# Performance work log

Hardware: AMD Instinct MI355X
Metric: run time of the kernel (lower is better)

Reference implementation:

```python
import jax, jax.numpy as jnp
import numpy as np

B = 8192
D_LS, D_A, D_LM, D_AT, D_DS, D_DM = 1024, 512, 512, 512, 1024, 512
LENGTH = D_LS + D_A + D_LM  # 2048
OUT = 512


def setup_inputs() -> dict:
    key = jax.random.key(0)
    ks = jax.random.split(key, 9)
    return {
        "result_ls": jax.random.normal(ks[0], (B, 1, D_LS), jnp.float32),
        "result_A": jax.random.normal(ks[1], (B, 1, D_A), jnp.float32),
        "result_lm": jax.random.normal(ks[2], (B, 1, D_LM), jnp.float32),
        "result_AT": jax.random.normal(ks[3], (B, 1, D_AT), jnp.float32),
        "result_ds": jax.random.normal(ks[4], (B, 1, D_DS), jnp.float32),
        "result_dm": jax.random.normal(ks[5], (B, 1, D_DM), jnp.float32),
        "W": jax.random.normal(ks[6], (OUT, LENGTH), jnp.float32) * (1.0 / np.sqrt(LENGTH)),
        "b": jax.random.normal(ks[7], (OUT,), jnp.float32) * 0.01,
        "h_n": jax.random.normal(ks[8], (OUT, 1), jnp.float32) * (1.0 / np.sqrt(OUT)),
    }


def _pad_to(x, length):
    # zero-pad last dim of [B,1,d] to [B,1,length]
    return jnp.pad(x, ((0, 0), (0, 0), (0, length - x.shape[2])))


def reference(result_ls, result_A, result_lm, result_AT, result_ds, result_dm, W, b, h_n):
    # pad each node-type feature to common length and stack along node axis -> [B,6,L]
    nodes = jnp.concatenate(
        [_pad_to(t, LENGTH) for t in (result_ls, result_A, result_lm, result_AT, result_ds, result_dm)],
        axis=1,
    )
    temp = jnp.tanh(jnp.einsum("bnl,ol->bno", nodes, W) + b)  # [B,6,OUT]
    score = jnp.einsum("bno,oi->bni", temp, h_n)               # [B,6,1]
    score = score.reshape(-1, 1, 6)
    beta = jax.nn.softmax(score, axis=2)                        # [B,1,6]
    z_i = jnp.matmul(beta, nodes)                               # [B,1,L]
    return z_i
```

## Files before the change

kernel.cpp:

```cpp
#include <hip/hip_runtime.h>
#include <hip/hip_bf16.h>
#include <stdint.h>

typedef __attribute__((ext_vector_type(8))) short bf16x8;
typedef __attribute__((ext_vector_type(4))) float f32x4;

#define NB 8192

__device__ __forceinline__ unsigned pkbf(float x, float y) {
    __hip_bfloat162 h = __float22bfloat162_rn(make_float2(x, y));
    unsigned r;
    __builtin_memcpy(&r, &h, 4);
    return r;
}

__device__ __forceinline__ uint4 pack8(float4 a, float4 b) {
    uint4 r;
    r.x = pkbf(a.x, a.y);
    r.y = pkbf(a.z, a.w);
    r.z = pkbf(b.x, b.y);
    r.w = pkbf(b.z, b.w);
    return r;
}

__global__ __launch_bounds__(256)
void prep_w_kernel(const float* __restrict__ W, uint4* __restrict__ Wt) {
    int t = blockIdx.x * 256 + threadIdx.x;
    int lane = t & 63;
    int frag = t >> 6;
    int kb = frag >> 5, cb = frag & 31;
    int o = cb * 16 + (lane & 15);
    int k = kb * 32 + ((lane >> 4) << 3);
    const float* src = W + (size_t)o * 2048 + k;
    float4 a = *(const float4*)src;
    float4 b = *(const float4*)(src + 4);
    Wt[t] = pack8(a, b);
}

template<int MFN, int DN>
__device__ __forceinline__ void score_body(
        const float* __restrict__ xp, int node, int m0,
        const float* __restrict__ bias, const float* __restrict__ hvec,
        const uint4* __restrict__ Wt, float* __restrict__ scores,
        uint4* lA, float* red) {
    constexpr int BM = MFN * 16;
    constexpr int NKB = DN / 32;
    int t = threadIdx.x;
    int l = t & 63;
    int w = t >> 6;

#pragma unroll
    for (int j = 0; j < 16; ++j) {
        int f = (t >> 6) + j * 8;
        int kb = f / MFN, mf = f % MFN;
        int row = mf * 16 + (l & 15);
        int k = kb * 32 + ((l >> 4) << 3);
        const float* g = xp + (size_t)(m0 + row) * DN + k;
        float4 a = *(const float4*)g;
        float4 b = *(const float4*)(g + 4);
        lA[f * 64 + l] = pack8(a, b);
    }
    __syncthreads();

    f32x4 acc[MFN][4];
#pragma unroll
    for (int mf = 0; mf < MFN; ++mf)
#pragma unroll
        for (int nf = 0; nf < 4; ++nf)
            acc[mf][nf] = (f32x4){0.f, 0.f, 0.f, 0.f};

    bf16x8 bcur[4];
    {
        const uint4* wp = Wt + ((0 + (w << 2)) << 6) + l;
#pragma unroll
        for (int nf = 0; nf < 4; ++nf) {
            uint4 u = wp[nf << 6];
            __builtin_memcpy(&bcur[nf], &u, 16);
        }
    }
    for (int kb = 0; kb < NKB; ++kb) {
        bf16x8 bnxt[4];
        if (kb + 1 < NKB) {
            const uint4* wp = Wt + ((((kb + 1) << 5) + (w << 2)) << 6) + l;
#pragma unroll
            for (int nf = 0; nf < 4; ++nf) {
                uint4 u = wp[nf << 6];
                __builtin_memcpy(&bnxt[nf], &u, 16);
            }
        }
#pragma unroll
        for (int mf = 0; mf < MFN; ++mf) {
            uint4 u = lA[(kb * MFN + mf) * 64 + l];
            bf16x8 afr;
            __builtin_memcpy(&afr, &u, 16);
#pragma unroll
            for (int nf = 0; nf < 4; ++nf)
                acc[mf][nf] = __builtin_amdgcn_mfma_f32_16x16x32_bf16(
                    afr, bcur[nf], acc[mf][nf], 0, 0, 0);
        }
#pragma unroll
        for (int nf = 0; nf < 4; ++nf) bcur[nf] = bnxt[nf];
    }

    float bv[4], hv[4];
#pragma unroll
    for (int nf = 0; nf < 4; ++nf) {
        int o = (w << 6) + (nf << 4) + (l & 15);
        bv[nf] = bias[o];
        hv[nf] = hvec[o];
    }
#pragma unroll
    for (int mf = 0; mf < MFN; ++mf) {
        float sc[4] = {0.f, 0.f, 0.f, 0.f};
#pragma unroll
        for (int nf = 0; nf < 4; ++nf) {
#pragma unroll
            for (int r = 0; r < 4; ++r) {
                float xv = acc[mf][nf][r] + bv[nf];
                float th = 1.f - 2.f * __builtin_amdgcn_rcpf(1.f + __expf(2.f * xv));
                sc[r] = fmaf(hv[nf], th, sc[r]);
            }
        }
#pragma unroll
        for (int r = 0; r < 4; ++r) {
            float v = sc[r];
            v += __shfl_xor(v, 1);
            v += __shfl_xor(v, 2);
            v += __shfl_xor(v, 4);
            v += __shfl_xor(v, 8);
            if ((l & 15) == 0)
                red[w * BM + (mf << 4) + ((l >> 4) << 2) + r] = v;
        }
    }
    __syncthreads();
    if (t < BM) {
        float ssum = 0.f;
#pragma unroll
        for (int w2 = 0; w2 < 8; ++w2) ssum += red[w2 * BM + t];
        scores[node * NB + m0 + t] = ssum;
    }
}

__global__ __launch_bounds__(512, 2)
void score_kernel(const float* __restrict__ x0, const float* __restrict__ x1,
                  const float* __restrict__ x2, const float* __restrict__ x3,
                  const float* __restrict__ x4, const float* __restrict__ x5,
                  const float* __restrict__ bias, const float* __restrict__ hvec,
                  const uint4* __restrict__ Wt, float* __restrict__ scores) {
    __shared__ uint4 lA[8192];
    __shared__ float red[8 * 128];

    int bid = blockIdx.x;
    if (bid < 256) {
        const float* xp = (bid & 1) ? x4 : x0;
        int node = (bid & 1) ? 4 : 0;
        int m0 = (bid >> 1) * 64;
        score_body<4, 1024>(xp, node, m0, bias, hvec, Wt, scores, lA, red);
    } else {
        int lb = bid - 256;
        int ni = lb & 3;
        const float* xp = (ni == 0) ? x1 : (ni == 1) ? x2 : (ni == 2) ? x3 : x5;
        int node = (ni == 0) ? 1 : (ni == 1) ? 2 : (ni == 2) ? 3 : 5;
        int m0 = (lb >> 2) * 128;
        score_body<8, 512>(xp, node, m0, bias, hvec, Wt, scores, lA, red);
    }
}

__global__ __launch_bounds__(256)
void z_kernel(const float* __restrict__ x0, const float* __restrict__ x1,
              const float* __restrict__ x2, const float* __restrict__ x3,
              const float* __restrict__ x4, const float* __restrict__ x5,
              const float* __restrict__ scores, float* __restrict__ out) {
    int wv = threadIdx.x >> 6;
    int lane = threadIdx.x & 63;
    int b = (blockIdx.x << 2) + wv;

    float s0 = scores[b];
    float s1 = scores[NB + b];
    float s2 = scores[2 * NB + b];
    float s3 = scores[3 * NB + b];
    float s4 = scores[4 * NB + b];
    float s5 = scores[5 * NB + b];
    float m = fmaxf(fmaxf(fmaxf(s0, s1), fmaxf(s2, s3)), fmaxf(s4, s5));
    float e0 = __expf(s0 - m), e1 = __expf(s1 - m), e2 = __expf(s2 - m);
    float e3 = __expf(s3 - m), e4 = __expf(s4 - m), e5 = __expf(s5 - m);
    float inv = __builtin_amdgcn_rcpf(e0 + e1 + e2 + e3 + e4 + e5);
    float b0 = e0 * inv, b1 = e1 * inv, b2 = e2 * inv;
    float b3 = e3 * inv, b4 = e4 * inv, b5 = e5 * inv;

    const float* pls = x0 + (size_t)b * 1024;
    const float* pA  = x1 + (size_t)b * 512;
    const float* plm = x2 + (size_t)b * 512;
    const float* pAT = x3 + (size_t)b * 512;
    const float* pds = x4 + (size_t)b * 1024;
    const float* pdm = x5 + (size_t)b * 512;
    float* po = out + (size_t)b * 2048;

#pragma unroll
    for (int j = 0; j < 2; ++j) {
        int c = (j << 8) + (lane << 2);
        float4 vls = *(const float4*)(pls + c);
        float4 vA  = *(const float4*)(pA + c);
        float4 vlm = *(const float4*)(plm + c);
        float4 vAT = *(const float4*)(pAT + c);
        float4 vds = *(const float4*)(pds + c);
        float4 vdm = *(const float4*)(pdm + c);
        float4 r;
        r.x = b0*vls.x + b1*vA.x + b2*vlm.x + b3*vAT.x + b4*vds.x + b5*vdm.x;
        r.y = b0*vls.y + b1*vA.y + b2*vlm.y + b3*vAT.y + b4*vds.y + b5*vdm.y;
        r.z = b0*vls.z + b1*vA.z + b2*vlm.z + b3*vAT.z + b4*vds.z + b5*vdm.z;
        r.w = b0*vls.w + b1*vA.w + b2*vlm.w + b3*vAT.w + b4*vds.w + b5*vdm.w;
        *(float4*)(po + c) = r;
    }
#pragma unroll
    for (int j = 0; j < 2; ++j) {
        int c = 512 + (j << 8) + (lane << 2);
        float4 vls = *(const float4*)(pls + c);
        float4 vds = *(const float4*)(pds + c);
        float4 r;
        r.x = b0*vls.x + b4*vds.x;
        r.y = b0*vls.y + b4*vds.y;
        r.z = b0*vls.z + b4*vds.z;
        r.w = b0*vls.w + b4*vds.w;
        *(float4*)(po + c) = r;
    }
    float4 zz = make_float4(0.f, 0.f, 0.f, 0.f);
#pragma unroll
    for (int j = 0; j < 4; ++j) {
        int c = 1024 + (j << 8) + (lane << 2);
        *(float4*)(po + c) = zz;
    }
}

extern "C" void kernel_launch(void* const* d_in, const int* in_sizes, int n_in,
                              void* d_out, int out_size, void* d_ws, size_t ws_size,
                              hipStream_t stream) {
    const float* x0   = (const float*)d_in[0];
    const float* x1   = (const float*)d_in[1];
    const float* x2   = (const float*)d_in[2];
    const float* x3   = (const float*)d_in[3];
    const float* x4   = (const float*)d_in[4];
    const float* x5   = (const float*)d_in[5];
    const float* W    = (const float*)d_in[6];
    const float* bias = (const float*)d_in[7];
    const float* hvec = (const float*)d_in[8];

    uint4* Wt = (uint4*)d_ws;
    float* scores = (float*)((char*)d_ws + (1u << 20));

    prep_w_kernel<<<256, 256, 0, stream>>>(W, Wt);
    score_kernel<<<512, 512, 0, stream>>>(x0, x1, x2, x3, x4, x5, bias, hvec, Wt, scores);
    z_kernel<<<2048, 256, 0, stream>>>(x0, x1, x2, x3, x4, x5, scores, (float*)d_out);
}
```

Baseline: 94.36 us.

## Pre-pack activations to bf16 fragment layout and stream them into LDS asynchronously

A new pre-pass converts all six activation tensors to bf16 in MFMA fragment order in the workspace. The score kernel then copies tiles straight into LDS with global_load_lds, uses 64-row tiles with half the LDS, and raises occupancy to 4 blocks per CU over 768 blocks. The aim is to take the fp32 conversion and scattered loads off the GEMM's critical path and raise occupancy. The cost is an extra 32 MB bf16 write and read-back, and the W-fragment prefetch double buffering is dropped. The old path is kept as a fallback when the workspace is too small.

New measurement: 131.3 us. +39.2%, slower.

```diff
diff --git a/kernel.cpp b/kernel.cpp
--- a/kernel.cpp
+++ b/kernel.cpp
@@ -21,6 +21,12 @@
     r.z = pkbf(b.x, b.y);
     r.w = pkbf(b.z, b.w);
     return r;
+}
+
+__device__ __forceinline__ void gload16(const uint4* g, void* l) {
+    __builtin_amdgcn_global_load_lds(
+        (const __attribute__((address_space(1))) void*)g,
+        (__attribute__((address_space(3))) void*)l, 16, 0, 0);
 }
 
 __global__ __launch_bounds__(256)
@@ -32,13 +38,149 @@
     int o = cb * 16 + (lane & 15);
     int k = kb * 32 + ((lane >> 4) << 3);
     const float* src = W + (size_t)o * 2048 + k;
-    float4 a = *(const float4*)src;
-    float4 b = *(const float4*)(src + 4);
-    Wt[t] = pack8(a, b);
+    Wt[t] = pack8(*(const float4*)src, *(const float4*)(src + 4));
+}
+
+__global__ __launch_bounds__(256)
+void prep_a_kernel(const float* __restrict__ x0, const float* __restrict__ x1,
+                   const float* __restrict__ x2, const float* __restrict__ x3,
+                   const float* __restrict__ x4, const float* __restrict__ x5,
+                   uint4* __restrict__ A) {
+    int c = blockIdx.x * 256 + threadIdx.x;
+    int s = c >> 19;
+    const float* xp; int dn, cn, cshift;
+    if (s < 2)      { xp = x0; dn = 1024; cn = c;                 cshift = 13; }
+    else if (s == 2){ xp = x1; dn = 512;  cn = c - (2 << 19);     cshift = 12; }
+    else if (s == 3){ xp = x2; dn = 512;  cn = c - (3 << 19);     cshift = 12; }
+    else if (s == 4){ xp = x3; dn = 512;  cn = c - (4 << 19);     cshift = 12; }
+    else if (s < 7) { xp = x4; dn = 1024; cn = c - (5 << 19);     cshift = 13; }
+    else            { xp = x5; dn = 512;  cn = c - (7 << 19);     cshift = 12; }
+    int tile = cn >> cshift;
+    int cc = cn & ((1 << cshift) - 1);
+    int f = cc >> 6, l = cc & 63;
+    int kb = f >> 2, mf = f & 3;
+    int row = (tile << 6) + (mf << 4) + (l & 15);
+    int k = (kb << 5) + ((l >> 4) << 3);
+    const float* src = xp + (size_t)row * dn + k;
+    A[c] = pack8(*(const float4*)src, *(const float4*)(src + 4));
+}
+
+template<int DN>
+__device__ __forceinline__ void score_v10_body(
+        const uint4* __restrict__ an, int node, int tile,
+        const float* __restrict__ bias, const float* __restrict__ hvec,
+        const uint4* __restrict__ Wt, float* __restrict__ scores,
+        uint4* lA, float* red) {
+    constexpr int NKH = DN / 512;
+    constexpr int CPT = DN * 8;
+    int t = threadIdx.x;
+    int l = t & 63;
+    int w = t >> 6;
+
+    f32x4 acc[4][4];
+#pragma unroll
+    for (int mf = 0; mf < 4; ++mf)
+#pragma unroll
+        for (int nf = 0; nf < 4; ++nf)
+            acc[mf][nf] = (f32x4){0.f, 0.f, 0.f, 0.f};
+
+    const uint4* tbase = an + (size_t)tile * CPT;
+
+    for (int kh = 0; kh < NKH; ++kh) {
+        if (kh > 0) __syncthreads();
+        {
+            const uint4* sb = tbase + (kh << 12) + (w << 9);
+            char* db = (char*)lA + ((w << 9) << 4);
+#pragma unroll
+            for (int i = 0; i < 8; ++i)
+                gload16(sb + (i << 6) + l, db + (i << 10));
+        }
+        __syncthreads();
+
+        for (int kbh = 0; kbh < 16; ++kbh) {
+            int kb = (kh << 4) + kbh;
+            const uint4* wp = Wt + (((kb << 5) + (w << 2)) << 6) + l;
+            bf16x8 bfr[4];
+#pragma unroll
+            for (int nf = 0; nf < 4; ++nf) {
+                uint4 u = wp[nf << 6];
+                __builtin_memcpy(&bfr[nf], &u, 16);
+            }
+#pragma unroll
+            for (int mf = 0; mf < 4; ++mf) {
+                uint4 u = lA[(((kbh << 2) + mf) << 6) + l];
+                bf16x8 afr;
+                __builtin_memcpy(&afr, &u, 16);
+#pragma unroll
+                for (int nf = 0; nf < 4; ++nf)
+                    acc[mf][nf] = __builtin_amdgcn_mfma_f32_16x16x32_bf16(
+                        afr, bfr[nf], acc[mf][nf], 0, 0, 0);
+            }
+        }
+    }
+
+    float bv[4], hv[4];
+#pragma unroll
+    for (int nf = 0; nf < 4; ++nf) {
+        int o = (w << 6) + (nf << 4) + (l & 15);
+        bv[nf] = bias[o];
+        hv[nf] = hvec[o];
+    }
+#pragma unroll
+    for (int mf = 0; mf < 4; ++mf) {
+        float sc[4] = {0.f, 0.f, 0.f, 0.f};
+#pragma unroll
+        for (int nf = 0; nf < 4; ++nf) {
+#pragma unroll
+            for (int r = 0; r < 4; ++r) {
+                float xv = acc[mf][nf][r] + bv[nf];
+                float th = 1.f - 2.f * __builtin_amdgcn_rcpf(1.f + __expf(2.f * xv));
+                sc[r] = fmaf(hv[nf], th, sc[r]);
+            }
+        }
+#pragma unroll
+        for (int r = 0; r < 4; ++r) {
+            float v = sc[r];
+            v += __shfl_xor(v, 1);
+            v += __shfl_xor(v, 2);
+            v += __shfl_xor(v, 4);
+            v += __shfl_xor(v, 8);
+            if ((l & 15) == 0)
+                red[(w << 6) + (mf << 4) + ((l >> 4) << 2) + r] = v;
+        }
+    }
+    __syncthreads();
+    if (t < 64) {
+        float ssum = 0.f;
+#pragma unroll
+        for (int w2 = 0; w2 < 8; ++w2) ssum += red[(w2 << 6) + t];
+        scores[node * NB + (tile << 6) + t] = ssum;
+    }
+}
+
+__global__ __launch_bounds__(512, 4)
+void score_v10_kernel(const uint4* __restrict__ a0, const uint4* __restrict__ a1,
+                      const uint4* __restrict__ a2, const uint4* __restrict__ a3,
+                      const uint4* __restrict__ a4, const uint4* __restrict__ a5,
+                      const float* __restrict__ bias, const float* __restrict__ hvec,
+                      const uint4* __restrict__ Wt, float* __restrict__ scores) {
+    __shared__ uint4 lA[4096];
+    __shared__ float red[8 * 64];
+    int bid = blockIdx.x;
+    int node = bid % 6;
+    int tile = bid / 6;
+    switch (node) {
+        case 0: score_v10_body<1024>(a0, 0, tile, bias, hvec, Wt, scores, lA, red); break;
+        case 1: score_v10_body<512>(a1, 1, tile, bias, hvec, Wt, scores, lA, red); break;
+        case 2: score_v10_body<512>(a2, 2, tile, bias, hvec, Wt, scores, lA, red); break;
+        case 3: score_v10_body<512>(a3, 3, tile, bias, hvec, Wt, scores, lA, red); break;
+        case 4: score_v10_body<1024>(a4, 4, tile, bias, hvec, Wt, scores, lA, red); break;
+        default: score_v10_body<512>(a5, 5, tile, bias, hvec, Wt, scores, lA, red); break;
+    }
 }
 
 template<int MFN, int DN>
-__device__ __forceinline__ void score_body(
+__device__ __forceinline__ void fb_score_body(
         const float* __restrict__ xp, int node, int m0,
         const float* __restrict__ bias, const float* __restrict__ hvec,
         const uint4* __restrict__ Wt, float* __restrict__ scores,
@@ -48,7 +190,6 @@
     int t = threadIdx.x;
     int l = t & 63;
     int w = t >> 6;
-
 #pragma unroll
     for (int j = 0; j < 16; ++j) {
         int f = (t >> 6) + j * 8;
@@ -56,37 +197,22 @@
         int row = mf * 16 + (l & 15);
         int k = kb * 32 + ((l >> 4) << 3);
         const float* g = xp + (size_t)(m0 + row) * DN + k;
-        float4 a = *(const float4*)g;
-        float4 b = *(const float4*)(g + 4);
-        lA[f * 64 + l] = pack8(a, b);
+        lA[f * 64 + l] = pack8(*(const float4*)g, *(const float4*)(g + 4));
     }
     __syncthreads();
-
     f32x4 acc[MFN][4];
 #pragma unroll
     for (int mf = 0; mf < MFN; ++mf)
 #pragma unroll
         for (int nf = 0; nf < 4; ++nf)
             acc[mf][nf] = (f32x4){0.f, 0.f, 0.f, 0.f};
-
-    bf16x8 bcur[4];
-    {
-        const uint4* wp = Wt + ((0 + (w << 2)) << 6) + l;
+    for (int kb = 0; kb < NKB; ++kb) {
+        bf16x8 bfr[4];
+        const uint4* wp = Wt + (((kb << 5) + (w << 2)) << 6) + l;
 #pragma unroll
         for (int nf = 0; nf < 4; ++nf) {
             uint4 u = wp[nf << 6];
-            __builtin_memcpy(&bcur[nf], &u, 16);
-        }
-    }
-    for (int kb = 0; kb < NKB; ++kb) {
-        bf16x8 bnxt[4];
-        if (kb + 1 < NKB) {
-            const uint4* wp = Wt + ((((kb + 1) << 5) + (w << 2)) << 6) + l;
-#pragma unroll
-            for (int nf = 0; nf < 4; ++nf) {
-                uint4 u = wp[nf << 6];
-                __builtin_memcpy(&bnxt[nf], &u, 16);
-            }
+            __builtin_memcpy(&bfr[nf], &u, 16);
         }
 #pragma unroll
         for (int mf = 0; mf < MFN; ++mf) {
@@ -96,12 +222,9 @@
 #pragma unroll
             for (int nf = 0; nf < 4; ++nf)
                 acc[mf][nf] = __builtin_amdgcn_mfma_f32_16x16x32_bf16(
-                    afr, bcur[nf], acc[mf][nf], 0, 0, 0);
-        }
-#pragma unroll
-        for (int nf = 0; nf < 4; ++nf) bcur[nf] = bnxt[nf];
-    }
-
+                    afr, bfr[nf], acc[mf][nf], 0, 0, 0);
+        }
+    }
     float bv[4], hv[4];
 #pragma unroll
     for (int nf = 0; nf < 4; ++nf) {
@@ -113,14 +236,13 @@
     for (int mf = 0; mf < MFN; ++mf) {
         float sc[4] = {0.f, 0.f, 0.f, 0.f};
 #pragma unroll
-        for (int nf = 0; nf < 4; ++nf) {
+        for (int nf = 0; nf < 4; ++nf)
 #pragma unroll
             for (int r = 0; r < 4; ++r) {
                 float xv = acc[mf][nf][r] + bv[nf];
                 float th = 1.f - 2.f * __builtin_amdgcn_rcpf(1.f + __expf(2.f * xv));
                 sc[r] = fmaf(hv[nf], th, sc[r]);
             }
-        }
 #pragma unroll
         for (int r = 0; r < 4; ++r) {
             float v = sc[r];
@@ -142,27 +264,26 @@
 }
 
 __global__ __launch_bounds__(512, 2)
-void score_kernel(const float* __restrict__ x0, const float* __restrict__ x1,
-                  const float* __restrict__ x2, const float* __restrict__ x3,
-                  const float* __restrict__ x4, const float* __restrict__ x5,
-                  const float* __restrict__ bias, const float* __restrict__ hvec,
-                  const uint4* __restrict__ Wt, float* __restrict__ scores) {
+void fb_score_kernel(const float* __restrict__ x0, const float* __restrict__ x1,
+                     const float* __restrict__ x2, const float* __restrict__ x3,
+                     const float* __restrict__ x4, const float* __restrict__ x5,
+                     const float* __restrict__ bias, const float* __restrict__ hvec,
+                     const uint4* __restrict__ Wt, float* __restrict__ scores) {
     __shared__ uint4 lA[8192];
     __shared__ float red[8 * 128];
-
     int bid = blockIdx.x;
     if (bid < 256) {
         const float* xp = (bid & 1) ? x4 : x0;
         int node = (bid & 1) ? 4 : 0;
         int m0 = (bid >> 1) * 64;
-        score_body<4, 1024>(xp, node, m0, bias, hvec, Wt, scores, lA, red);
+        fb_score_body<4, 1024>(xp, node, m0, bias, hvec, Wt, scores, lA, red);
     } else {
         int lb = bid - 256;
         int ni = lb & 3;
         const float* xp = (ni == 0) ? x1 : (ni == 1) ? x2 : (ni == 2) ? x3 : x5;
         int node = (ni == 0) ? 1 : (ni == 1) ? 2 : (ni == 2) ? 3 : 5;
         int m0 = (lb >> 2) * 128;
-        score_body<8, 512>(xp, node, m0, bias, hvec, Wt, scores, lA, red);
+        fb_score_body<8, 512>(xp, node, m0, bias, hvec, Wt, scores, lA, red);
     }
 }
 
@@ -247,8 +368,23 @@
 
     uint4* Wt = (uint4*)d_ws;
     float* scores = (float*)((char*)d_ws + (1u << 20));
+    uint4* A = (uint4*)((char*)d_ws + (2u << 20));
+    size_t need = (size_t)(2u << 20) + ((size_t)64 << 20);
 
     prep_w_kernel<<<256, 256, 0, stream>>>(W, Wt);
-    score_kernel<<<512, 512, 0, stream>>>(x0, x1, x2, x3, x4, x5, bias, hvec, Wt, scores);
+    if (ws_size >= need) {
+        prep_a_kernel<<<16384, 256, 0, stream>>>(x0, x1, x2, x3, x4, x5, A);
+        const uint4* a0 = A;
+        const uint4* a1 = A + (2u << 19);
+        const uint4* a2 = A + (3u << 19);
+        const uint4* a3 = A + (4u << 19);
+        const uint4* a4 = A + (5u << 19);
+        const uint4* a5 = A + (7u << 19);
+        score_v10_kernel<<<768, 512, 0, stream>>>(a0, a1, a2, a3, a4, a5,
+                                                  bias, hvec, Wt, scores);
+    } else {
+        fb_score_kernel<<<512, 512, 0, stream>>>(x0, x1, x2, x3, x4, x5,
+                                                 bias, hvec, Wt, scores);
+    }
     z_kernel<<<2048, 256, 0, stream>>>(x0, x1, x2, x3, x4, x5, scores, (float*)d_out);
 }
```
